# Performance work log

Measured on AMD Instinct MI355X. Metric: run time of the kernel, lower is better.

Reference implementation:

```python
import jax, jax.numpy as jnp
import numpy as np

B, N, O, K, F = 4, 256, 5, 5, 256
H, D, DFF = 4, 64, 1024  # num_heads, KQ_len, FFN hidden
EPS = 1e-5


def setup_inputs() -> dict:
    key = jax.random.key(0)
    ks = jax.random.split(key, 16)
    s = 0.05
    p = lambda k, shape: (jax.random.normal(k, shape, jnp.float32) * s)
    return {
        "x": jax.random.normal(ks[0], (B, N, O, K, K, F), jnp.float32),
        "Wq": p(ks[1], (H * D, F)), "bq": p(ks[2], (H * D,)),
        "Wk": p(ks[3], (H * D, F)), "bk": p(ks[4], (H * D,)),
        "Wv": p(ks[5], (H * D, F)), "bv": p(ks[6], (H * D,)),
        "Wf": p(ks[7], (F, F)), "bf": p(ks[8], (F,)),
        "ln1_w": jnp.ones((N, O, F), jnp.float32), "ln1_b": jnp.zeros((N, O, F), jnp.float32),
        "ln2_w": jnp.ones((N, O, F), jnp.float32), "ln2_b": jnp.zeros((N, O, F), jnp.float32),
        "W1": p(ks[9], (DFF, F)), "b1": p(ks[10], (DFF,)),
        "W2": p(ks[11], (F, DFF)), "b2": p(ks[12], (F,)),
    }


def _layer_norm3(x, w, b):
    # torch LayerNorm with normalized_shape=[N, O, F]: stats over last 3 dims
    mu = jnp.mean(x, axis=(1, 2, 3), keepdims=True)
    var = jnp.var(x, axis=(1, 2, 3), keepdims=True)
    return (x - mu) * jax.lax.rsqrt(var + EPS) * w + b


def _split_heads(y):
    # [B,N,O,K,K,H*D] -> [B,N,O,H,K,K,D]
    return y.reshape(B, N, O, K, K, H, D).transpose(0, 1, 2, 5, 3, 4, 6)


def reference(x, Wq, bq, Wk, bk, Wv, bv, Wf, bf,
              ln1_w, ln1_b, ln2_w, ln2_b, W1, b1, W2, b2):
    q = _split_heads(x @ Wq.T + bq)
    k = _split_heads(x @ Wk.T + bk)
    v = _split_heads(x @ Wv.T + bv)
    c = K // 2
    qc = q[:, :, :, :, c, c, :]  # center query [B,N,O,H,D]
    # tile+mul+sum == dot of center query against every patch key
    scores = jnp.einsum('bnohd,bnohijd->bnohij', qc, k) / np.sqrt(float(D))
    w = jax.nn.softmax(scores.reshape(B, N, O, H, K * K), axis=-1)
    merged = jnp.einsum('bnohp,bnohpd->bnohd', w, v.reshape(B, N, O, H, K * K, D))
    merged = merged.reshape(B, N, O, H * D)
    attent = merged @ Wf.T + bf  # dropout = identity (eval)
    out1 = _layer_norm3(attent, ln1_w, ln1_b)
    ffn = jax.nn.relu(out1 @ W1.T + b1) @ W2.T + b2
    return _layer_norm3(out1 + ffn, ln2_w, ln2_b)
```

## Files before the change

kernel.cpp:

```cpp
#include <hip/hip_runtime.h>
#include <hip/hip_bf16.h>

#define FF 256
#define HH 4
#define DD 64
#define PP 25
#define SITES 5120
#define SPB 1280
#define DFF 1024
#define LN_ELEMS 327680

typedef const __hip_bfloat16* bfp;
typedef __hip_bfloat16* bfw;
typedef __attribute__((ext_vector_type(8))) short bf16x8;
typedef __attribute__((ext_vector_type(4))) float f32x4;

__device__ __forceinline__ float b2f(const __hip_bfloat16 v) { return __bfloat162float(v); }
__device__ __forceinline__ bool detect_bf(const unsigned* dt) {
    return dt[0] == 0x3F803F80u;
}
__device__ __forceinline__ float ldin(const void* p, size_t i, bool bf) {
    return bf ? __bfloat162float(((const __hip_bfloat16*)p)[i]) : ((const float*)p)[i];
}
__device__ __forceinline__ unsigned short f2bu(float f) {
    __hip_bfloat16 h = __float2bfloat16(f);
    return *(unsigned short*)&h;
}
__device__ __forceinline__ uint4 ldin8(const void* p, size_t i, bool bf) {
    if (bf) return *(const uint4*)((const unsigned short*)p + i);
    const float* f = (const float*)p + i;
    const float4 a = *(const float4*)f;
    const float4 b = *(const float4*)(f + 4);
    unsigned short u[8] = { f2bu(a.x), f2bu(a.y), f2bu(a.z), f2bu(a.w),
                            f2bu(b.x), f2bu(b.y), f2bu(b.z), f2bu(b.w) };
    return *(uint4*)u;
}
__device__ __forceinline__ void ldraw8(const void* p, size_t i, bool bf, uint4& lo, uint4& hi) {
    if (bf) { lo = *(const uint4*)((const unsigned short*)p + i); return; }
    const float* f = (const float*)p + i;
    lo = *(const uint4*)f;
    hi = *(const uint4*)(f + 4);
}
__device__ __forceinline__ uint4 cvt8(bool bf, uint4 lo, uint4 hi) {
    if (bf) return lo;
    const float* a = (const float*)&lo;
    const float* b = (const float*)&hi;
    unsigned short u[8] = { f2bu(a[0]), f2bu(a[1]), f2bu(a[2]), f2bu(a[3]),
                            f2bu(b[0]), f2bu(b[1]), f2bu(b[2]), f2bu(b[3]) };
    return *(uint4*)u;
}

template<int RELU, int RES, int GATHER, int STATS, int BINT>
__global__ __launch_bounds__(256) void gemm_mfma(
    const void* xg, bfp Ab, int lda,
    const void* Bm, int ldb, const void* bias,
    bfp resid, int ldr, bfw C, int ldc, int Kc,
    int aoh, size_t boh, int bioh, int coh,
    float* __restrict__ red, const unsigned* dt)
{
    const bool bf = detect_bf(dt);
    const int h = blockIdx.z;
    Ab += (size_t)h * aoh;
    const size_t boff = (size_t)h * boh;
    const size_t biasoff = (size_t)h * bioh;
    C += (size_t)h * coh;

    __shared__ unsigned short Als[64][72];
    __shared__ unsigned short Bls[64][72];
    __shared__ float rs4[4], rss4[4];
    const int tid = threadIdx.x;
    const int lane = tid & 63;
    const int w = tid >> 6;
    const int m0 = blockIdx.y * 64;
    const int n0 = blockIdx.x * 64;
    const int r8 = tid >> 3;
    const int c8 = (tid & 7) * 8;

    f32x4 acc[4];
    #pragma unroll
    for (int mi = 0; mi < 4; ++mi) acc[mi] = (f32x4){0.f, 0.f, 0.f, 0.f};

    uint4 aLo0, aHi0, aLo1, aHi1, bLo0, bHi0, bLo1, bHi1;
    auto fetch = [&](int kk) {
        if (GATHER) {
            ldraw8(xg, ((size_t)(m0 + r8) * PP + 12) * FF + (kk + c8), bf, aLo0, aHi0);
            ldraw8(xg, ((size_t)(m0 + r8 + 32) * PP + 12) * FF + (kk + c8), bf, aLo1, aHi1);
        } else {
            aLo0 = *(const uint4*)(Ab + (size_t)(m0 + r8) * lda + (kk + c8));
            aLo1 = *(const uint4*)(Ab + (size_t)(m0 + r8 + 32) * lda + (kk + c8));
        }
        if (BINT) {
            bLo0 = *(const uint4*)((const unsigned short*)Bm + boff + (size_t)(n0 + r8) * ldb + (kk + c8));
            bLo1 = *(const uint4*)((const unsigned short*)Bm + boff + (size_t)(n0 + r8 + 32) * ldb + (kk + c8));
        } else {
            ldraw8(Bm, boff + (size_t)(n0 + r8) * ldb + (kk + c8), bf, bLo0, bHi0);
            ldraw8(Bm, boff + (size_t)(n0 + r8 + 32) * ldb + (kk + c8), bf, bLo1, bHi1);
        }
    };
    fetch(0);

    for (int k0 = 0; k0 < Kc; k0 += 64) {
        *(uint4*)&Als[r8][c8]      = GATHER ? cvt8(bf, aLo0, aHi0) : aLo0;
        *(uint4*)&Als[r8 + 32][c8] = GATHER ? cvt8(bf, aLo1, aHi1) : aLo1;
        *(uint4*)&Bls[r8][c8]      = BINT ? bLo0 : cvt8(bf, bLo0, bHi0);
        *(uint4*)&Bls[r8 + 32][c8] = BINT ? bLo1 : cvt8(bf, bLo1, bHi1);
        __syncthreads();
        if (k0 + 64 < Kc) fetch(k0 + 64);
        #pragma unroll
        for (int ks = 0; ks < 2; ++ks) {
            const int kq = ks * 32 + (lane >> 4) * 8;
            const bf16x8 bfr = *(const bf16x8*)&Bls[w * 16 + (lane & 15)][kq];
            #pragma unroll
            for (int mi = 0; mi < 4; ++mi) {
                const bf16x8 afr = *(const bf16x8*)&Als[mi * 16 + (lane & 15)][kq];
                acc[mi] = __builtin_amdgcn_mfma_f32_16x16x32_bf16(afr, bfr, acc[mi], 0, 0, 0);
            }
        }
        __syncthreads();
    }

    const int col = n0 + w * 16 + (lane & 15);
    const int quad = lane >> 4;
    const float bvv = bias ? (BINT ? ((const float*)bias)[biasoff + col]
                                   : ldin(bias, biasoff + col, bf)) : 0.f;
    float s_ = 0.f, ss_ = 0.f;
    #pragma unroll
    for (int mi = 0; mi < 4; ++mi) {
        #pragma unroll
        for (int r = 0; r < 4; ++r) {
            const int row = m0 + mi * 16 + quad * 4 + r;
            float v = acc[mi][r] + bvv;
            if (RES)  v += b2f(resid[(size_t)row * ldr + col]);
            if (RELU) v = fmaxf(v, 0.0f);
            if (STATS) { s_ += v; ss_ += v * v; }
            C[(size_t)row * ldc + col] = __float2bfloat16(v);
        }
    }
    if (STATS) {
        #pragma unroll
        for (int o = 32; o > 0; o >>= 1) { s_ += __shfl_down(s_, o); ss_ += __shfl_down(ss_, o); }
        if (lane == 0) { rs4[w] = s_; rss4[w] = ss_; }
        __syncthreads();
        if (tid == 0) {
            const int batch = m0 / SPB;
            atomicAdd(&red[batch * 2 + 0], rs4[0] + rs4[1] + rs4[2] + rs4[3]);
            atomicAdd(&red[batch * 2 + 1], rss4[0] + rss4[1] + rss4[2] + rss4[3]);
        }
    }
}

__global__ __launch_bounds__(256) void prep(
    const void* Wq, const void* Wk, const void* Wv, const void* Wf,
    const void* bq, const void* bv, const void* bfv,
    bfw WqT, bfw WkT, bfw WvT, bfw WfB,
    float* __restrict__ rh, float* __restrict__ cf, const unsigned* dt)
{
    const bool bf = detect_bf(dt);
    const int bid = blockIdx.x;
    const int t = threadIdx.x;
    if (bid < 1024) {
        const int gid = bid * 256 + t;
        const int sec = gid >> 16;
        const int i = gid & 65535;
        if (sec == 3) { WfB[i] = __float2bfloat16(ldin(Wf, i, bf)); return; }
        const int d = i & 63, f = (i >> 6) & 255, h = i >> 14;
        const void* W = sec == 0 ? Wq : sec == 1 ? Wk : Wv;
        bfw WT = sec == 0 ? WqT : sec == 1 ? WkT : WvT;
        WT[i] = __float2bfloat16(ldin(W, (size_t)(h * DD + d) * FF + f, bf));
        return;
    }
    if (bid < 1028) {
        const int h = bid - 1024;
        float acc = 0.f;
        for (int d = 0; d < DD; ++d)
            acc += ldin(bq, h * DD + d, bf) * ldin(Wk, (size_t)(h * DD + d) * FF + t, bf);
        rh[h * FF + t] = acc;
        return;
    }
    float acc = ldin(bfv, t, bf);
    for (int j = 0; j < FF; ++j)
        acc += ldin(Wf, (size_t)t * FF + j, bf) * ldin(bv, j, bf);
    cf[t] = acc;
}

__global__ __launch_bounds__(256) void attn_site(const void* x, bfp qk, bfw xw,
                                                 const unsigned* dt)
{
    __shared__ unsigned short xsb[32][264];
    __shared__ unsigned short qkb[HH][FF];
    __shared__ float sc[HH][32];
    __shared__ float wl[HH][PP];

    const bool bf = detect_bf(dt);
    const int s = blockIdx.x;
    const int t = threadIdx.x;

    const size_t xbase = (size_t)s * (PP * FF);
    for (int e0 = t * 8; e0 < PP * FF; e0 += 2048)
        *(uint4*)&xsb[e0 >> 8][e0 & 255] = ldin8(x, xbase + e0, bf);
    if (t < 128)
        ((uint4*)qkb)[t] = ((const uint4*)(qk + (size_t)s * (HH * FF)))[t];
    __syncthreads();

    if (t < 64) {
        const int lane = t;
        const int col = lane & 15;
        const int quad = lane >> 4;
        const int brow = col & 3;
        f32x4 a0v = (f32x4){0.f, 0.f, 0.f, 0.f};
        f32x4 a1v = (f32x4){0.f, 0.f, 0.f, 0.f};
        #pragma unroll
        for (int ks = 0; ks < 8; ++ks) {
            const int kq = ks * 32 + quad * 8;
            const bf16x8 bfr = *(const bf16x8*)&qkb[brow][kq];
            const bf16x8 af0 = *(const bf16x8*)&xsb[col][kq];
            const bf16x8 af1 = *(const bf16x8*)&xsb[16 + col][kq];
            a0v = __builtin_amdgcn_mfma_f32_16x16x32_bf16(af0, bfr, a0v, 0, 0, 0);
            a1v = __builtin_amdgcn_mfma_f32_16x16x32_bf16(af1, bfr, a1v, 0, 0, 0);
        }
        if (col < HH) {
            #pragma unroll
            for (int r = 0; r < 4; ++r) {
                const int p = quad * 4 + r;
                sc[col][p] = a0v[r] * 0.125f;
                const int p2 = 16 + p;
                if (p2 < PP) sc[col][p2] = a1v[r] * 0.125f;
            }
        }
    }
    __syncthreads();

    if (t < HH) {
        float m = -1e30f;
        #pragma unroll
        for (int p = 0; p < PP; ++p) m = fmaxf(m, sc[t][p]);
        float e[PP], ssum = 0.f;
        #pragma unroll
        for (int p = 0; p < PP; ++p) { e[p] = __expf(sc[t][p] - m); ssum += e[p]; }
        const float inv = 1.f / ssum;
        #pragma unroll
        for (int p = 0; p < PP; ++p) wl[t][p] = e[p] * inv;
    }
    __syncthreads();

    float a0 = 0.f, a1 = 0.f, a2 = 0.f, a3 = 0.f;
    #pragma unroll
    for (int p = 0; p < PP; ++p) {
        const float xv = __bfloat162float(*(const __hip_bfloat16*)&xsb[p][t]);
        a0 = fmaf(wl[0][p], xv, a0);
        a1 = fmaf(wl[1][p], xv, a1);
        a2 = fmaf(wl[2][p], xv, a2);
        a3 = fmaf(wl[3][p], xv, a3);
    }
    bfw xwp = xw + (size_t)s * (HH * FF) + t;
    xwp[0 * FF] = __float2bfloat16(a0);
    xwp[1 * FF] = __float2bfloat16(a1);
    xwp[2 * FF] = __float2bfloat16(a2);
    xwp[3 * FF] = __float2bfloat16(a3);
}

template<int FINAL>
__global__ __launch_bounds__(256) void ln_apply(bfp X, const float* __restrict__ red,
                                                const void* w, const void* b,
                                                void* out, const unsigned* dt)
{
    const bool bf = detect_bf(dt);
    const int i8 = (blockIdx.x * 256 + threadIdx.x) * 8;
    const int s = i8 >> 8;
    const int batch = s / SPB;
    const int r = s - batch * SPB;
    const int f = i8 & 255;
    const float inv = 1.f / (float)LN_ELEMS;
    const float mu = red[batch * 2] * inv;
    const float var = red[batch * 2 + 1] * inv - mu * mu;
    const float rs = rsqrtf(var + 1e-5f);

    const uint4 xv = *(const uint4*)(X + i8);
    const uint4 wv = ldin8(w, (size_t)r * FF + f, bf);
    const uint4 bv = ldin8(b, (size_t)r * FF + f, bf);
    const unsigned short* xu = (const unsigned short*)&xv;
    const unsigned short* wu = (const unsigned short*)&wv;
    const unsigned short* bu = (const unsigned short*)&bv;
    float vo[8];
    #pragma unroll
    for (int j = 0; j < 8; ++j) {
        const float xf = __bfloat162float(*(const __hip_bfloat16*)&xu[j]);
        const float wf = __bfloat162float(*(const __hip_bfloat16*)&wu[j]);
        const float bf2 = __bfloat162float(*(const __hip_bfloat16*)&bu[j]);
        vo[j] = (xf - mu) * rs * wf + bf2;
    }
    if (FINAL && !bf) {
        float* o = (float*)out + i8;
        *(float4*)o = (float4){vo[0], vo[1], vo[2], vo[3]};
        *(float4*)(o + 4) = (float4){vo[4], vo[5], vo[6], vo[7]};
    } else {
        unsigned short ou[8];
        #pragma unroll
        for (int j = 0; j < 8; ++j) ou[j] = f2bu(vo[j]);
        *(uint4*)((unsigned short*)out + i8) = *(uint4*)ou;
    }
}

extern "C" void kernel_launch(void* const* d_in, const int* in_sizes, int n_in,
                              void* d_out, int out_size, void* d_ws, size_t ws_size,
                              hipStream_t stream)
{
    const void* x    = d_in[0];
    const void* Wq   = d_in[1];
    const void* bq   = d_in[2];
    const void* Wk   = d_in[3];
    const void* Wv   = d_in[5];
    const void* bv   = d_in[6];
    const void* Wf   = d_in[7];
    const void* bfv  = d_in[8];
    const void* ln1w = d_in[9];
    const void* ln1b = d_in[10];
    const void* ln2w = d_in[11];
    const void* ln2b = d_in[12];
    const void* W1   = d_in[13];
    const void* b1   = d_in[14];
    const void* W2   = d_in[15];
    const void* b2   = d_in[16];
    const unsigned* dt = (const unsigned*)d_in[9];

    char* w8 = (char*)d_ws;
    bfw qk   = (bfw)(w8);
    bfw xw   = (bfw)(w8 + 10485760);
    bfw hid  = (bfw)(w8 + 20971520);
    bfw WqT  = (bfw)(w8 + 31457280);
    bfw WkT  = (bfw)(w8 + 31588352);
    bfw WvT  = (bfw)(w8 + 31719424);
    bfw WfB  = (bfw)(w8 + 31850496);
    bfw Mt   = (bfw)(w8 + 31981568);
    bfw Bvf  = (bfw)(w8 + 32505856);
    bfw att  = (bfw)(w8 + 33030144);
    bfw out1 = (bfw)(w8 + 35651584);
    bfw z    = (bfw)(w8 + 38273024);
    float* rh  = (float*)(w8 + 40894464);
    float* cf  = (float*)(w8 + 40898560);
    float* red = (float*)(w8 + 40899584);

    hipMemsetAsync(red, 0, 64, stream);

    prep<<<1029, 256, 0, stream>>>(Wq, Wk, Wv, Wf, bq, bv, bfv,
                                   WqT, WkT, WvT, WfB, rh, cf, dt);

    gemm_mfma<0, 0, 0, 0, 1><<<dim3(4, 4, HH), 256, 0, stream>>>(
        nullptr, WkT, DD, WqT, DD, nullptr, nullptr, 0, Mt, FF, DD,
        FF * DD, (size_t)FF * DD, 0, FF * FF, nullptr, dt);

    gemm_mfma<0, 0, 0, 0, 1><<<dim3(4, 4, HH), 256, 0, stream>>>(
        nullptr, WfB, FF, WvT, DD, nullptr, nullptr, 0, Bvf, HH * FF, DD,
        DD, (size_t)FF * DD, 0, FF, nullptr, dt);

    gemm_mfma<0, 0, 1, 0, 1><<<dim3(4, 80, HH), 256, 0, stream>>>(
        x, nullptr, 0, Mt, FF, rh, nullptr, 0, qk, HH * FF, FF,
        0, (size_t)FF * FF, FF, FF, nullptr, dt);

    attn_site<<<SITES, 256, 0, stream>>>(x, qk, xw, dt);

    gemm_mfma<0, 0, 0, 1, 1><<<dim3(4, 80), 256, 0, stream>>>(
        nullptr, xw, HH * FF, Bvf, HH * FF, cf, nullptr, 0, att, FF, HH * FF,
        0, 0, 0, 0, red, dt);

    ln_apply<0><<<640, 256, 0, stream>>>(att, red, ln1w, ln1b, out1, dt);

    gemm_mfma<1, 0, 0, 0, 0><<<dim3(16, 80), 256, 0, stream>>>(
        nullptr, out1, FF, W1, FF, b1, nullptr, 0, hid, DFF, FF,
        0, 0, 0, 0, nullptr, dt);

    gemm_mfma<0, 1, 0, 1, 0><<<dim3(4, 80), 256, 0, stream>>>(
        nullptr, hid, DFF, W2, DFF, b2, out1, FF, z, FF, DFF,
        0, 0, 0, 0, red + 8, dt);

    ln_apply<1><<<640, 256, 0, stream>>>(z, red + 8, ln2w, ln2b, d_out, dt);
}
```

Before: 350.6 us.

## Fuse LN1 into FFN GEMMs, fold weight premultiply into prep, warp-parallel softmax

The first LayerNorm is no longer materialised. It is applied on the fly while loading the A tile of the first FFN GEMM, and again in the epilogue of the second FFN GEMM for the residual. This removes the ln_apply kernel and the out1 buffer round-trip. The separate weight transposes and the two small per-head GEMMs that built Mt and Bvf are replaced by direct dot products inside the prep kernel, and the QK GEMM now runs with all heads in one grid, cutting several launches. The attention softmax moves from 4 serial threads to 32-lane shuffle reductions, at the cost of recomputing LN weights and normalisation per column block.

```diff
diff --git a/kernel.cpp b/kernel.cpp
--- a/kernel.cpp
+++ b/kernel.cpp
@@ -50,21 +50,15 @@
     return *(uint4*)u;
 }
 
-template<int RELU, int RES, int GATHER, int STATS, int BINT>
+template<int RELU, int RES, int GATHER, int STATS, int BINT, int LNA>
 __global__ __launch_bounds__(256) void gemm_mfma(
     const void* xg, bfp Ab, int lda,
     const void* Bm, int ldb, const void* bias,
     bfp resid, int ldr, bfw C, int ldc, int Kc,
-    int aoh, size_t boh, int bioh, int coh,
+    const float* __restrict__ lnred, const void* lnw, const void* lnb,
     float* __restrict__ red, const unsigned* dt)
 {
     const bool bf = detect_bf(dt);
-    const int h = blockIdx.z;
-    Ab += (size_t)h * aoh;
-    const size_t boff = (size_t)h * boh;
-    const size_t biasoff = (size_t)h * bioh;
-    C += (size_t)h * coh;
-
     __shared__ unsigned short Als[64][72];
     __shared__ unsigned short Bls[64][72];
     __shared__ float rs4[4], rss4[4];
@@ -76,6 +70,17 @@
     const int r8 = tid >> 3;
     const int c8 = (tid & 7) * 8;
 
+    float mu1 = 0.f, rstd1 = 0.f;
+    int r1base = 0;
+    if (LNA || RES == 2) {
+        const int batch = m0 / SPB;
+        r1base = m0 - batch * SPB;
+        const float inv = 1.f / (float)LN_ELEMS;
+        mu1 = lnred[batch * 2] * inv;
+        const float var = lnred[batch * 2 + 1] * inv - mu1 * mu1;
+        rstd1 = rsqrtf(var + 1e-5f);
+    }
+
     f32x4 acc[4];
     #pragma unroll
     for (int mi = 0; mi < 4; ++mi) acc[mi] = (f32x4){0.f, 0.f, 0.f, 0.f};
@@ -90,18 +95,41 @@
             aLo1 = *(const uint4*)(Ab + (size_t)(m0 + r8 + 32) * lda + (kk + c8));
         }
         if (BINT) {
-            bLo0 = *(const uint4*)((const unsigned short*)Bm + boff + (size_t)(n0 + r8) * ldb + (kk + c8));
-            bLo1 = *(const uint4*)((const unsigned short*)Bm + boff + (size_t)(n0 + r8 + 32) * ldb + (kk + c8));
+            bLo0 = *(const uint4*)((const unsigned short*)Bm + (size_t)(n0 + r8) * ldb + (kk + c8));
+            bLo1 = *(const uint4*)((const unsigned short*)Bm + (size_t)(n0 + r8 + 32) * ldb + (kk + c8));
         } else {
-            ldraw8(Bm, boff + (size_t)(n0 + r8) * ldb + (kk + c8), bf, bLo0, bHi0);
-            ldraw8(Bm, boff + (size_t)(n0 + r8 + 32) * ldb + (kk + c8), bf, bLo1, bHi1);
+            ldraw8(Bm, (size_t)(n0 + r8) * ldb + (kk + c8), bf, bLo0, bHi0);
+            ldraw8(Bm, (size_t)(n0 + r8 + 32) * ldb + (kk + c8), bf, bLo1, bHi1);
         }
     };
     fetch(0);
 
     for (int k0 = 0; k0 < Kc; k0 += 64) {
-        *(uint4*)&Als[r8][c8]      = GATHER ? cvt8(bf, aLo0, aHi0) : aLo0;
-        *(uint4*)&Als[r8 + 32][c8] = GATHER ? cvt8(bf, aLo1, aHi1) : aLo1;
+        if (LNA) {
+            #pragma unroll
+            for (int rr = 0; rr < 2; ++rr) {
+                const int row = r8 + rr * 32;
+                const uint4 av = rr ? aLo1 : aLo0;
+                const size_t wi = (size_t)(r1base + row) * FF + (k0 + c8);
+                const uint4 wv = ldin8(lnw, wi, bf);
+                const uint4 bv2 = ldin8(lnb, wi, bf);
+                const unsigned short* au = (const unsigned short*)&av;
+                const unsigned short* wu = (const unsigned short*)&wv;
+                const unsigned short* bu = (const unsigned short*)&bv2;
+                unsigned short o[8];
+                #pragma unroll
+                for (int j = 0; j < 8; ++j) {
+                    const float xv = __bfloat162float(*(const __hip_bfloat16*)&au[j]);
+                    const float wf = __bfloat162float(*(const __hip_bfloat16*)&wu[j]);
+                    const float bb = __bfloat162float(*(const __hip_bfloat16*)&bu[j]);
+                    o[j] = f2bu((xv - mu1) * rstd1 * wf + bb);
+                }
+                *(uint4*)&Als[row][c8] = *(uint4*)o;
+            }
+        } else {
+            *(uint4*)&Als[r8][c8]      = GATHER ? cvt8(bf, aLo0, aHi0) : aLo0;
+            *(uint4*)&Als[r8 + 32][c8] = GATHER ? cvt8(bf, aLo1, aHi1) : aLo1;
+        }
         *(uint4*)&Bls[r8][c8]      = BINT ? bLo0 : cvt8(bf, bLo0, bHi0);
         *(uint4*)&Bls[r8 + 32][c8] = BINT ? bLo1 : cvt8(bf, bLo1, bHi1);
         __syncthreads();
@@ -121,8 +149,8 @@
 
     const int col = n0 + w * 16 + (lane & 15);
     const int quad = lane >> 4;
-    const float bvv = bias ? (BINT ? ((const float*)bias)[biasoff + col]
-                                   : ldin(bias, biasoff + col, bf)) : 0.f;
+    const float bvv = bias ? (BINT ? ((const float*)bias)[col]
+                                   : ldin(bias, col, bf)) : 0.f;
     float s_ = 0.f, ss_ = 0.f;
     #pragma unroll
     for (int mi = 0; mi < 4; ++mi) {
@@ -130,7 +158,13 @@
         for (int r = 0; r < 4; ++r) {
             const int row = m0 + mi * 16 + quad * 4 + r;
             float v = acc[mi][r] + bvv;
-            if (RES)  v += b2f(resid[(size_t)row * ldr + col]);
+            if (RES == 1) v += b2f(resid[(size_t)row * ldr + col]);
+            if (RES == 2) {
+                const int r1 = r1base + (row - m0);
+                const float av = b2f(resid[(size_t)row * ldr + col]);
+                v += (av - mu1) * rstd1 * ldin(lnw, (size_t)r1 * FF + col, bf)
+                     + ldin(lnb, (size_t)r1 * FF + col, bf);
+            }
             if (RELU) v = fmaxf(v, 0.0f);
             if (STATS) { s_ += v; ss_ += v * v; }
             C[(size_t)row * ldc + col] = __float2bfloat16(v);
@@ -152,28 +186,40 @@
 __global__ __launch_bounds__(256) void prep(
     const void* Wq, const void* Wk, const void* Wv, const void* Wf,
     const void* bq, const void* bv, const void* bfv,
-    bfw WqT, bfw WkT, bfw WvT, bfw WfB,
-    float* __restrict__ rh, float* __restrict__ cf, const unsigned* dt)
+    bfw Mt, bfw Bvf, float* __restrict__ rh, float* __restrict__ cf,
+    const unsigned* dt)
 {
     const bool bf = detect_bf(dt);
     const int bid = blockIdx.x;
     const int t = threadIdx.x;
     if (bid < 1024) {
-        const int gid = bid * 256 + t;
-        const int sec = gid >> 16;
-        const int i = gid & 65535;
-        if (sec == 3) { WfB[i] = __float2bfloat16(ldin(Wf, i, bf)); return; }
-        const int d = i & 63, f = (i >> 6) & 255, h = i >> 14;
-        const void* W = sec == 0 ? Wq : sec == 1 ? Wk : Wv;
-        bfw WT = sec == 0 ? WqT : sec == 1 ? WkT : WvT;
-        WT[i] = __float2bfloat16(ldin(W, (size_t)(h * DD + d) * FF + f, bf));
+        const int h = bid >> 8, f = bid & 255;
+        float acc = 0.f;
+        #pragma unroll 8
+        for (int d = 0; d < DD; ++d)
+            acc += ldin(Wk, (size_t)(h * DD + d) * FF + f, bf)
+                 * ldin(Wq, (size_t)(h * DD + d) * FF + t, bf);
+        Mt[(size_t)bid * FF + t] = __float2bfloat16(acc);
         return;
     }
-    if (bid < 1028) {
-        const int h = bid - 1024;
+    if (bid < 2048) {
+        const int b2 = bid - 1024;
+        const int g = b2 >> 2, h = b2 & 3;
         float acc = 0.f;
+        #pragma unroll 8
         for (int d = 0; d < DD; ++d)
-            acc += ldin(bq, h * DD + d, bf) * ldin(Wk, (size_t)(h * DD + d) * FF + t, bf);
+            acc += ldin(Wf, (size_t)g * FF + h * DD + d, bf)
+                 * ldin(Wv, (size_t)(h * DD + d) * FF + t, bf);
+        Bvf[(size_t)g * (HH * FF) + h * FF + t] = __float2bfloat16(acc);
+        return;
+    }
+    if (bid < 2052) {
+        const int h = bid - 2048;
+        float acc = 0.f;
+        #pragma unroll 8
+        for (int d = 0; d < DD; ++d)
+            acc += ldin(bq, h * DD + d, bf)
+                 * ldin(Wk, (size_t)(h * DD + d) * FF + t, bf);
         rh[h * FF + t] = acc;
         return;
     }
@@ -230,16 +276,17 @@
     }
     __syncthreads();
 
-    if (t < HH) {
-        float m = -1e30f;
-        #pragma unroll
-        for (int p = 0; p < PP; ++p) m = fmaxf(m, sc[t][p]);
-        float e[PP], ssum = 0.f;
-        #pragma unroll
-        for (int p = 0; p < PP; ++p) { e[p] = __expf(sc[t][p] - m); ssum += e[p]; }
-        const float inv = 1.f / ssum;
-        #pragma unroll
-        for (int p = 0; p < PP; ++p) wl[t][p] = e[p] * inv;
+    if (t < 128) {
+        const int hh = t >> 5, p = t & 31;
+        const float sv = (p < PP) ? sc[hh][p] : -1e30f;
+        float m = sv;
+        #pragma unroll
+        for (int o = 16; o > 0; o >>= 1) m = fmaxf(m, __shfl_xor(m, o, 32));
+        const float e = (p < PP) ? __expf(sv - m) : 0.f;
+        float ssum = e;
+        #pragma unroll
+        for (int o = 16; o > 0; o >>= 1) ssum += __shfl_xor(ssum, o, 32);
+        if (p < PP) wl[hh][p] = e / ssum;
     }
     __syncthreads();
 
@@ -327,51 +374,36 @@
     bfw qk   = (bfw)(w8);
     bfw xw   = (bfw)(w8 + 10485760);
     bfw hid  = (bfw)(w8 + 20971520);
-    bfw WqT  = (bfw)(w8 + 31457280);
-    bfw WkT  = (bfw)(w8 + 31588352);
-    bfw WvT  = (bfw)(w8 + 31719424);
-    bfw WfB  = (bfw)(w8 + 31850496);
-    bfw Mt   = (bfw)(w8 + 31981568);
-    bfw Bvf  = (bfw)(w8 + 32505856);
-    bfw att  = (bfw)(w8 + 33030144);
-    bfw out1 = (bfw)(w8 + 35651584);
-    bfw z    = (bfw)(w8 + 38273024);
-    float* rh  = (float*)(w8 + 40894464);
-    float* cf  = (float*)(w8 + 40898560);
-    float* red = (float*)(w8 + 40899584);
+    bfw Mt   = (bfw)(w8 + 31457280);
+    bfw Bvf  = (bfw)(w8 + 31981568);
+    bfw att  = (bfw)(w8 + 32505856);
+    bfw z    = (bfw)(w8 + 35127296);
+    float* rh  = (float*)(w8 + 37748736);
+    float* cf  = (float*)(w8 + 37752832);
+    float* red = (float*)(w8 + 37753856);
 
     hipMemsetAsync(red, 0, 64, stream);
 
-    prep<<<1029, 256, 0, stream>>>(Wq, Wk, Wv, Wf, bq, bv, bfv,
-                                   WqT, WkT, WvT, WfB, rh, cf, dt);
-
-    gemm_mfma<0, 0, 0, 0, 1><<<dim3(4, 4, HH), 256, 0, stream>>>(
-        nullptr, WkT, DD, WqT, DD, nullptr, nullptr, 0, Mt, FF, DD,
-        FF * DD, (size_t)FF * DD, 0, FF * FF, nullptr, dt);
-
-    gemm_mfma<0, 0, 0, 0, 1><<<dim3(4, 4, HH), 256, 0, stream>>>(
-        nullptr, WfB, FF, WvT, DD, nullptr, nullptr, 0, Bvf, HH * FF, DD,
-        DD, (size_t)FF * DD, 0, FF, nullptr, dt);
-
-    gemm_mfma<0, 0, 1, 0, 1><<<dim3(4, 80, HH), 256, 0, stream>>>(
+    prep<<<2053, 256, 0, stream>>>(Wq, Wk, Wv, Wf, bq, bv, bfv,
+                                   Mt, Bvf, rh, cf, dt);
+
+    gemm_mfma<0, 0, 1, 0, 1, 0><<<dim3(16, 80), 256, 0, stream>>>(
         x, nullptr, 0, Mt, FF, rh, nullptr, 0, qk, HH * FF, FF,
-        0, (size_t)FF * FF, FF, FF, nullptr, dt);
+        nullptr, nullptr, nullptr, nullptr, dt);
 
     attn_site<<<SITES, 256, 0, stream>>>(x, qk, xw, dt);
 
-    gemm_mfma<0, 0, 0, 1, 1><<<dim3(4, 80), 256, 0, stream>>>(
+    gemm_mfma<0, 0, 0, 1, 1, 0><<<dim3(4, 80), 256, 0, stream>>>(
         nullptr, xw, HH * FF, Bvf, HH * FF, cf, nullptr, 0, att, FF, HH * FF,
-        0, 0, 0, 0, red, dt);
-
-    ln_apply<0><<<640, 256, 0, stream>>>(att, red, ln1w, ln1b, out1, dt);
-
-    gemm_mfma<1, 0, 0, 0, 0><<<dim3(16, 80), 256, 0, stream>>>(
-        nullptr, out1, FF, W1, FF, b1, nullptr, 0, hid, DFF, FF,
-        0, 0, 0, 0, nullptr, dt);
-
-    gemm_mfma<0, 1, 0, 1, 0><<<dim3(4, 80), 256, 0, stream>>>(
-        nullptr, hid, DFF, W2, DFF, b2, out1, FF, z, FF, DFF,
-        0, 0, 0, 0, red + 8, dt);
+        nullptr, nullptr, nullptr, red, dt);
+
+    gemm_mfma<1, 0, 0, 0, 0, 1><<<dim3(16, 80), 256, 0, stream>>>(
+        nullptr, att, FF, W1, FF, b1, nullptr, 0, hid, DFF, FF,
+        red, ln1w, ln1b, nullptr, dt);
+
+    gemm_mfma<0, 2, 0, 1, 0, 0><<<dim3(4, 80), 256, 0, stream>>>(
+        nullptr, hid, DFF, W2, DFF, b2, att, FF, z, FF, DFF,
+        red, ln1w, ln1b, red + 8, dt);
 
     ln_apply<1><<<640, 256, 0, stream>>>(z, red + 8, ln2w, ln2b, d_out, dt);
 }
```

Measured after the change: 361.9 us. 3.2% more time.
